# Kernel tuning notes

Hardware: AMD Instinct MI355X
Metric: run time of the kernel (lower is better)

Reference implementation:

```python
import jax, jax.numpy as jnp
import numpy as np

N = 50000   # nodes
E = 800000  # edges (avg degree 16)
D = 128     # node latent dim
DE = 128    # edge latent dim
L = 3       # num_mp_steps


def setup_inputs() -> dict:
    key = jax.random.key(0)
    ks = jax.random.split(key, 10)
    s = 0.05
    return dict(
        x=jax.random.normal(ks[0], (N, D), jnp.float32),
        edge_index=jax.random.randint(ks[1], (2, E), 0, N, jnp.int32),
        edge_attr=jax.random.normal(ks[2], (E, DE), jnp.float32),
        # per-layer GATConv params (stacked over L layers)
        W=jax.random.normal(ks[3], (L, D, D), jnp.float32) * s,        # lin (shared src/dst)
        att_src=jax.random.normal(ks[4], (L, D), jnp.float32) * s,
        att_dst=jax.random.normal(ks[5], (L, D), jnp.float32) * s,
        W_e=jax.random.normal(ks[6], (L, DE, D), jnp.float32) * s,     # lin_edge
        att_edge=jax.random.normal(ks[7], (L, D), jnp.float32) * s,
        bias=jnp.zeros((L, D), jnp.float32),
        ln_gamma=jnp.ones((L, D), jnp.float32),                        # post-conv LayerNorm
        ln_beta=jnp.zeros((L, D), jnp.float32),
    )


def reference(x, edge_index, edge_attr, W, att_src, att_dst, W_e, att_edge, bias, ln_gamma, ln_beta):
    n = x.shape[0]
    src, dst = edge_index[0], edge_index[1]

    # add_self_loops with fill_value='mean': self-loop edge feature of node i is
    # the mean of raw edge features of edges incoming to i (0 if none).
    ones = jnp.ones((src.shape[0],), x.dtype)
    deg = jax.ops.segment_sum(ones, dst, num_segments=n)
    loop_attr = jax.ops.segment_sum(edge_attr, dst, num_segments=n) / jnp.maximum(deg, 1.0)[:, None]
    loop = jnp.arange(n, dtype=src.dtype)
    src_f = jnp.concatenate([src, loop])            # [E+N]
    dst_f = jnp.concatenate([dst, loop])            # [E+N]
    ea_f = jnp.concatenate([edge_attr, loop_attr], axis=0)  # [E+N, DE]

    def layer(h_in, p):
        Wl, asl, adl, Wel, ael, bl, gl, bel = p
        h = h_in @ Wl                                              # [N, D]
        # per-edge attention logits (heads=1)
        a = (h @ asl)[src_f] + (h @ adl)[dst_f] + ea_f @ (Wel @ ael)  # [E+N]
        a = jnp.where(a > 0, a, 0.2 * a)                           # LeakyReLU(0.2)
        # segment softmax over destination nodes (every node has a self loop)
        m = jax.ops.segment_max(a, dst_f, num_segments=n)
        ea = jnp.exp(a - m[dst_f])
        denom = jax.ops.segment_sum(ea, dst_f, num_segments=n)
        alpha = ea / denom[dst_f]
        out = jax.ops.segment_sum(h[src_f] * alpha[:, None], dst_f, num_segments=n) + bl
        # LayerNorm (elementwise affine)
        mu = jnp.mean(out, axis=-1, keepdims=True)
        var = jnp.var(out, axis=-1, keepdims=True)
        out = (out - mu) * jax.lax.rsqrt(var + 1e-5) * gl + bel
        return out, None

    h, _ = jax.lax.scan(layer, x, (W, att_src, att_dst, W_e, att_edge, bias, ln_gamma, ln_beta))
    return h
```

## Files before the change

kernel.cpp:

```cpp
#include <hip/hip_runtime.h>
#include <cstdint>

#define D 128
#define LNUM 3

typedef short short8 __attribute__((ext_vector_type(8)));
typedef float f32x4 __attribute__((ext_vector_type(4)));

static __device__ __forceinline__ float wred_sum(float x) {
#pragma unroll
    for (int off = 32; off; off >>= 1) x += __shfl_xor(x, off);
    return x;
}
static __device__ __forceinline__ float wred_max(float x) {
#pragma unroll
    for (int off = 32; off; off >>= 1) x = fmaxf(x, __shfl_xor(x, off));
    return x;
}
static __device__ __forceinline__ uint32_t f2bf_rne(float x) {
    uint32_t u = __float_as_uint(x);
    uint32_t r = u + 0x7fffu + ((u >> 16) & 1u);
    return r >> 16;
}


__global__ void hist_k(const int* __restrict__ dst, int* __restrict__ cnt, int E) {
    int e = blockIdx.x * blockDim.x + threadIdx.x;
    if (e < E) atomicAdd(&cnt[dst[e]], 1);
}

__global__ __launch_bounds__(1024) void scan_k(const int* __restrict__ cnt, int* __restrict__ rowptr, int N) {
    __shared__ int sh[1024];
    int t = threadIdx.x;
    int chunk = (N + 1023) >> 10;
    int b = t * chunk;
    int e = min(b + chunk, N);
    int s = 0;
    for (int i = b; i < e; ++i) s += cnt[i];
    sh[t] = s;
    __syncthreads();
    for (int off = 1; off < 1024; off <<= 1) {
        int v = (t >= off) ? sh[t - off] : 0;
        __syncthreads();
        sh[t] += v;
        __syncthreads();
    }
    int run = sh[t] - s;
    for (int i = b; i < e; ++i) { rowptr[i] = run; run += cnt[i]; }
    if (t == 1023) rowptr[N] = sh[1023];
}

__global__ void fill_k(const int* __restrict__ src, const int* __restrict__ dst,
                       const int* __restrict__ rowptr, int* __restrict__ cnt,
                       int* __restrict__ colA, int* __restrict__ pos, int E) {
    int e = blockIdx.x * blockDim.x + threadIdx.x;
    if (e >= E) return;
    int d = dst[e];
    int p = atomicAdd(&cnt[d], 1);
    int q = rowptr[d] + p;
    colA[q] = src[e];
    pos[e] = q;
}


__global__ __launch_bounds__(256) void prep_k(const float* __restrict__ We, const float* __restrict__ ae,
                                              const float* __restrict__ W, float* __restrict__ vbuf,
                                              uint16_t* __restrict__ Wt) {
    int l = blockIdx.x;
    int t = threadIdx.x;
    if (t < D) {
        const float* Wrow = We + ((size_t)l * D + t) * D;
        const float* a = ae + (size_t)l * D;
        float s = 0.f;
        for (int d = 0; d < D; ++d) s += Wrow[d] * a[d];
        vbuf[l * D + t] = s;
    }
    for (int i = t; i < D * D; i += 256) {
        int j = i >> 7, k = i & 127;
        Wt[(size_t)l * D * D + i] = (uint16_t)f2bf_rne(W[(size_t)l * D * D + (size_t)k * D + j]);
    }
}


__global__ __launch_bounds__(256) void cvt_k(const float* __restrict__ x, uint16_t* __restrict__ xb, int total4) {
    int i = blockIdx.x * blockDim.x + threadIdx.x;
    int stride = gridDim.x * blockDim.x;
    for (; i < total4; i += stride) {
        float4 v = *(const float4*)&x[(size_t)i * 4];
        uint2 o;
        o.x = f2bf_rne(v.x) | (f2bf_rne(v.y) << 16);
        o.y = f2bf_rne(v.z) | (f2bf_rne(v.w) << 16);
        *(uint2*)&xb[(size_t)i * 4] = o;
    }
}


__global__ __launch_bounds__(256) void ec_k(const float* __restrict__ ea, const float* __restrict__ vbuf,
                                            const int* __restrict__ pos, float* __restrict__ ecp, int E) {
    __shared__ float vs[3][D];
    int t = threadIdx.x;
    if (t < D) {
        vs[0][t] = vbuf[t];
        vs[1][t] = vbuf[D + t];
        vs[2][t] = vbuf[2 * D + t];
    }
    __syncthreads();
    int e = blockIdx.x * 32 + (t >> 3);
    int sub = t & 7;
    if (e >= E) return;
    const float* row = ea + (size_t)e * D + sub * 16;
    float p0 = 0.f, p1 = 0.f, p2 = 0.f;
#pragma unroll
    for (int i = 0; i < 4; ++i) {
        float4 v = *(const float4*)&row[i * 4];
        int c = sub * 16 + i * 4;
        p0 += v.x * vs[0][c] + v.y * vs[0][c + 1] + v.z * vs[0][c + 2] + v.w * vs[0][c + 3];
        p1 += v.x * vs[1][c] + v.y * vs[1][c + 1] + v.z * vs[1][c + 2] + v.w * vs[1][c + 3];
        p2 += v.x * vs[2][c] + v.y * vs[2][c + 1] + v.z * vs[2][c + 2] + v.w * vs[2][c + 3];
    }
#pragma unroll
    for (int off = 1; off < 8; off <<= 1) {
        p0 += __shfl_xor(p0, off);
        p1 += __shfl_xor(p1, off);
        p2 += __shfl_xor(p2, off);
    }
    if (sub == 0) {
        int q = pos[e];
        ecp[q] = p0;
        ecp[E + q] = p1;
        ecp[2 * (size_t)E + q] = p2;
    }
}


__global__ __launch_bounds__(256) void gemm_mfma_k(const uint16_t* __restrict__ A,
                                                   const uint16_t* __restrict__ Wt,
                                                   const float* __restrict__ as_,
                                                   const float* __restrict__ ad_,
                                                   uint16_t* __restrict__ hbf,
                                                   float* __restrict__ hs, float* __restrict__ hd, int N) {
    __shared__ uint4 As[64 * 16];
    int t = threadIdx.x;
    int row0 = blockIdx.x * 64;
#pragma unroll
    for (int it = 0; it < 4; ++it) {
        int idx = it * 256 + t;
        int r = idx >> 4, s = idx & 15;
        int gr = row0 + r;
        uint4 v = make_uint4(0u, 0u, 0u, 0u);
        if (gr < N) v = *(const uint4*)&A[(size_t)gr * D + s * 8];
        As[r * 16 + (s ^ (r & 7))] = v;
    }
    __syncthreads();
    int w = t >> 6, l = t & 63;
    int lrow = l & 15, lk = l >> 4;
    int rbase = w * 16;
    short8 afrag[4];
#pragma unroll
    for (int ks = 0; ks < 4; ++ks) {
        int r = rbase + lrow;
        int s = (ks * 4 + lk) ^ (r & 7);
        afrag[ks] = __builtin_bit_cast(short8, As[r * 16 + s]);
    }
    float psum[4] = {0.f, 0.f, 0.f, 0.f}, pdum[4] = {0.f, 0.f, 0.f, 0.f};
#pragma unroll
    for (int ct = 0; ct < 8; ++ct) {
        f32x4 acc = {0.f, 0.f, 0.f, 0.f};
#pragma unroll
        for (int ks = 0; ks < 4; ++ks) {
            short8 b = *(const short8*)&Wt[(size_t)(ct * 16 + lrow) * D + ks * 32 + lk * 8];
            acc = __builtin_amdgcn_mfma_f32_16x16x32_bf16(afrag[ks], b, acc, 0, 0, 0);
        }
        int col_g = ct * 16 + lrow;
        float av = as_[col_g], dv = ad_[col_g];
#pragma unroll
        for (int r = 0; r < 4; ++r) {
            float v = acc[r];
            psum[r] += v * av;
            pdum[r] += v * dv;
            int row_g = row0 + rbase + lk * 4 + r;
            if (row_g < N) hbf[(size_t)row_g * D + col_g] = (uint16_t)f2bf_rne(v);
        }
    }
#pragma unroll
    for (int r = 0; r < 4; ++r) {
        float ps = psum[r], pd = pdum[r];
#pragma unroll
        for (int off = 1; off < 16; off <<= 1) {
            ps += __shfl_xor(ps, off);
            pd += __shfl_xor(pd, off);
        }
        if (lrow == 0) {
            int row_g = row0 + rbase + lk * 4 + r;
            if (row_g < N) { hs[row_g] = ps; hd[row_g] = pd; }
        }
    }
}


__global__ __launch_bounds__(256) void node_k(const uint32_t* __restrict__ hb, const float* __restrict__ hs,
                                              const float* __restrict__ hd, const float* __restrict__ ecp,
                                              const int* __restrict__ rowptr, const int* __restrict__ colA,
                                              const float* __restrict__ bias, const float* __restrict__ gamma,
                                              const float* __restrict__ beta,
                                              uint32_t* __restrict__ outb, float* __restrict__ outf, int N) {
    __shared__ float s_al[4][66];
    __shared__ int s_co[4][66];
    int w = threadIdx.x >> 6;
    int lane = threadIdx.x & 63;
    int wid = blockIdx.x * 4 + w;
    if (wid >= N) return;
    int beg = rowptr[wid], end = rowptr[wid + 1];
    int deg = end - beg;
    float hdi = hd[wid];
    float hsi = hs[wid];
    float acc0 = 0.f, acc1 = 0.f;

    if (deg <= 63) {
        bool v = lane < deg;
        int col = v ? colA[beg + lane] : 0;
        float ec = v ? ecp[beg + lane] : 0.f;
        float a = v ? (hs[col] + hdi + ec) : -3e38f;
        a = a > 0.f ? a : 0.2f * a;
        float sumec = wred_sum(ec);
        float ecs = deg > 0 ? sumec / (float)deg : 0.f;
        float as_ = hsi + hdi + ecs;
        as_ = as_ > 0.f ? as_ : 0.2f * as_;
        float m = fmaxf(wred_max(a), as_);
        float p = __expf(a - m);
        float ps = __expf(as_ - m);
        float denom = wred_sum(p) + ps;
        float inv = 1.f / denom;
        s_al[w][lane] = p * inv;
        s_co[w][lane] = col;
        if (lane == 0) { s_al[w][deg] = ps * inv; s_co[w][deg] = wid; }
        __asm__ volatile("s_waitcnt lgkmcnt(0)" ::: "memory");
        int ne = deg + 1;
        int j = 0;
        for (; j + 4 <= ne; j += 4) {
            int c0 = s_co[w][j], c1 = s_co[w][j + 1], c2 = s_co[w][j + 2], c3 = s_co[w][j + 3];
            float a0 = s_al[w][j], a1 = s_al[w][j + 1], a2 = s_al[w][j + 2], a3 = s_al[w][j + 3];
            uint32_t b0 = hb[(size_t)c0 * 64 + lane];
            uint32_t b1 = hb[(size_t)c1 * 64 + lane];
            uint32_t b2 = hb[(size_t)c2 * 64 + lane];
            uint32_t b3 = hb[(size_t)c3 * 64 + lane];
            acc0 += a0 * __uint_as_float(b0 << 16) + a1 * __uint_as_float(b1 << 16) +
                    a2 * __uint_as_float(b2 << 16) + a3 * __uint_as_float(b3 << 16);
            acc1 += a0 * __uint_as_float(b0 & 0xffff0000u) + a1 * __uint_as_float(b1 & 0xffff0000u) +
                    a2 * __uint_as_float(b2 & 0xffff0000u) + a3 * __uint_as_float(b3 & 0xffff0000u);
        }
        for (; j < ne; ++j) {
            int c0 = s_co[w][j];
            float a0 = s_al[w][j];
            uint32_t b0 = hb[(size_t)c0 * 64 + lane];
            acc0 += a0 * __uint_as_float(b0 << 16);
            acc1 += a0 * __uint_as_float(b0 & 0xffff0000u);
        }
    } else {
        float m = -3e38f, dsum = 0.f, sumec = 0.f;
        for (int base = 0; base < deg; base += 64) {
            int j = base + lane;
            bool v = j < deg;
            int col = v ? colA[beg + j] : 0;
            float ec = v ? ecp[beg + j] : 0.f;
            float a = v ? (hs[col] + hdi + ec) : -3e38f;
            a = a > 0.f ? a : 0.2f * a;
            sumec += wred_sum(ec);
            float cm = wred_max(a);
            float nm = fmaxf(m, cm);
            dsum = dsum * __expf(m - nm) + wred_sum(__expf(a - nm));
            m = nm;
        }
        float ecs = sumec / (float)deg;
        float as_ = hsi + hdi + ecs;
        as_ = as_ > 0.f ? as_ : 0.2f * as_;
        float nm = fmaxf(m, as_);
        dsum = dsum * __expf(m - nm) + __expf(as_ - nm);
        m = nm;
        float inv = 1.f / dsum;
        for (int base = 0; base < deg; base += 64) {
            int j = base + lane;
            bool v = j < deg;
            int col = v ? colA[beg + j] : 0;
            float ec = v ? ecp[beg + j] : 0.f;
            float a = v ? (hs[col] + hdi + ec) : -3e38f;
            a = a > 0.f ? a : 0.2f * a;
            __asm__ volatile("s_waitcnt lgkmcnt(0)" ::: "memory");
            s_al[w][lane] = __expf(a - m) * inv;
            s_co[w][lane] = col;
            __asm__ volatile("s_waitcnt lgkmcnt(0)" ::: "memory");
            int cnt = min(64, deg - base);
            for (int k = 0; k < cnt; ++k) {
                int c = s_co[w][k];
                float al = s_al[w][k];
                uint32_t b = hb[(size_t)c * 64 + lane];
                acc0 += al * __uint_as_float(b << 16);
                acc1 += al * __uint_as_float(b & 0xffff0000u);
            }
        }
        float alS = __expf(as_ - m) * inv;
        uint32_t b = hb[(size_t)wid * 64 + lane];
        acc0 += alS * __uint_as_float(b << 16);
        acc1 += alS * __uint_as_float(b & 0xffff0000u);
    }

    float2 bi = *(const float2*)&bias[lane * 2];
    float o0 = acc0 + bi.x, o1 = acc1 + bi.y;
    float mean = wred_sum(o0 + o1) * (1.f / 128.f);
    float d0 = o0 - mean, d1 = o1 - mean;
    float var = wred_sum(d0 * d0 + d1 * d1) * (1.f / 128.f);
    float rstd = rsqrtf(var + 1e-5f);
    float2 g = *(const float2*)&gamma[lane * 2];
    float2 be = *(const float2*)&beta[lane * 2];
    float2 o;
    o.x = d0 * rstd * g.x + be.x;
    o.y = d1 * rstd * g.y + be.y;
    if (outf) {
        *(float2*)&outf[(size_t)wid * D + lane * 2] = o;
    } else {
        outb[(size_t)wid * 64 + lane] = f2bf_rne(o.x) | (f2bf_rne(o.y) << 16);
    }
}


extern "C" void kernel_launch(void* const* d_in, const int* in_sizes, int n_in,
                              void* d_out, int out_size, void* d_ws, size_t ws_size,
                              hipStream_t stream) {
    const float* x = (const float*)d_in[0];
    const int* ei = (const int*)d_in[1];
    const float* ea = (const float*)d_in[2];
    const float* W = (const float*)d_in[3];
    const float* att_src = (const float*)d_in[4];
    const float* att_dst = (const float*)d_in[5];
    const float* We = (const float*)d_in[6];
    const float* att_edge = (const float*)d_in[7];
    const float* bias = (const float*)d_in[8];
    const float* gamma = (const float*)d_in[9];
    const float* beta = (const float*)d_in[10];

    int N = in_sizes[0] / D;
    int E = in_sizes[1] / 2;
    const int* srcA = ei;
    const int* dstA = ei + E;

    float* p = (float*)d_ws;
    float* hsb = p;   p += N;
    float* hdb = p;   p += N;
    float* vbuf = p;  p += LNUM * D;
    float* ecp = p;   p += (size_t)LNUM * E;
    uint16_t* xb = (uint16_t*)p;
    uint16_t* hbf = xb + (size_t)N * D;
    uint16_t* hnb = hbf + (size_t)N * D;
    uint16_t* Wt = hnb + (size_t)N * D;
    int* ip = (int*)(Wt + (size_t)LNUM * D * D);
    int* rowptr = ip; ip += N + 1;
    int* cnt = ip;    ip += N;
    int* colA = ip;   ip += E;
    int* pos = ip;    ip += E;

    hipMemsetAsync(cnt, 0, sizeof(int) * N, stream);
    hist_k<<<(E + 255) / 256, 256, 0, stream>>>(dstA, cnt, E);
    scan_k<<<1, 1024, 0, stream>>>(cnt, rowptr, N);
    hipMemsetAsync(cnt, 0, sizeof(int) * N, stream);
    fill_k<<<(E + 255) / 256, 256, 0, stream>>>(srcA, dstA, rowptr, cnt, colA, pos, E);
    prep_k<<<LNUM, 256, 0, stream>>>(We, att_edge, W, vbuf, Wt);
    ec_k<<<(E + 31) / 32, 256, 0, stream>>>(ea, vbuf, pos, ecp, E);
    cvt_k<<<2048, 256, 0, stream>>>(x, xb, N * D / 4);

    const uint16_t* hin = xb;
    for (int l = 0; l < LNUM; ++l) {
        gemm_mfma_k<<<(N + 63) / 64, 256, 0, stream>>>(hin, Wt + (size_t)l * D * D,
                                                       att_src + (size_t)l * D, att_dst + (size_t)l * D,
                                                       hbf, hsb, hdb, N);
        bool last = (l == LNUM - 1);
        node_k<<<(N + 3) / 4, 256, 0, stream>>>((const uint32_t*)hbf, hsb, hdb, ecp + (size_t)l * E,
                                                rowptr, colA, bias + (size_t)l * D,
                                                gamma + (size_t)l * D, beta + (size_t)l * D,
                                                last ? nullptr : (uint32_t*)hnb,
                                                last ? (float*)d_out : nullptr, N);
        hin = hnb;
    }
}
```

Before: 489.0 us.

## Fuse preprocessing kernels and pack CSR column with per-layer edge scores

Merges the histogram, weight transpose/convert, edge-vector projection and x-to-bf16 conversion into one grid-stride kernel. The CSR fill is folded into the edge-score kernel by decrementing the histogram counts with atomicSub, which removes the second memset and the pos array. Column index and the three per-layer edge logits are packed into one 16-byte record per edge, so node_k does a single vector load per edge. This cuts launches and the scattered writes, but each layer now reads 16 bytes per edge instead of 8.

Result: faster. 431.4 us (-11.8%).

```diff
diff --git a/kernel.cpp b/kernel.cpp
--- a/kernel.cpp
+++ b/kernel.cpp
@@ -24,10 +24,38 @@
 }
 
 
-__global__ void hist_k(const int* __restrict__ dst, int* __restrict__ cnt, int E) {
-    int e = blockIdx.x * blockDim.x + threadIdx.x;
-    if (e < E) atomicAdd(&cnt[dst[e]], 1);
-}
+__global__ __launch_bounds__(256) void pre_k(const float* __restrict__ W, const float* __restrict__ We,
+                                             const float* __restrict__ ae, const float* __restrict__ x,
+                                             const int* __restrict__ dst,
+                                             uint16_t* __restrict__ Wt, float* __restrict__ vbuf,
+                                             uint16_t* __restrict__ xb, int* __restrict__ cnt,
+                                             int ND4, int E) {
+    int tid = blockIdx.x * 256 + threadIdx.x;
+    int stride = gridDim.x * 256;
+    for (int i = tid; i < ND4; i += stride) {
+        float4 v = *(const float4*)&x[(size_t)i * 4];
+        uint2 o;
+        o.x = f2bf_rne(v.x) | (f2bf_rne(v.y) << 16);
+        o.y = f2bf_rne(v.z) | (f2bf_rne(v.w) << 16);
+        *(uint2*)&xb[(size_t)i * 4] = o;
+    }
+    for (int e = tid; e < E; e += stride) atomicAdd(&cnt[dst[e]], 1);
+    for (int i = tid; i < LNUM * D * D; i += stride) {
+        int l = i >> 14;
+        int r = i & (D * D - 1);
+        int j = r >> 7, k = r & 127;
+        Wt[i] = (uint16_t)f2bf_rne(W[(size_t)l * D * D + (size_t)k * D + j]);
+    }
+    if (tid < LNUM * D) {
+        int l = tid >> 7, j = tid & 127;
+        const float* Wrow = We + ((size_t)l * D + j) * D;
+        const float* a = ae + (size_t)l * D;
+        float s = 0.f;
+        for (int d = 0; d < D; ++d) s += Wrow[d] * a[d];
+        vbuf[tid] = s;
+    }
+}
+
 
 __global__ __launch_bounds__(1024) void scan_k(const int* __restrict__ cnt, int* __restrict__ rowptr, int N) {
     __shared__ int sh[1024];
@@ -50,53 +78,11 @@
     if (t == 1023) rowptr[N] = sh[1023];
 }
 
-__global__ void fill_k(const int* __restrict__ src, const int* __restrict__ dst,
-                       const int* __restrict__ rowptr, int* __restrict__ cnt,
-                       int* __restrict__ colA, int* __restrict__ pos, int E) {
-    int e = blockIdx.x * blockDim.x + threadIdx.x;
-    if (e >= E) return;
-    int d = dst[e];
-    int p = atomicAdd(&cnt[d], 1);
-    int q = rowptr[d] + p;
-    colA[q] = src[e];
-    pos[e] = q;
-}
-
-
-__global__ __launch_bounds__(256) void prep_k(const float* __restrict__ We, const float* __restrict__ ae,
-                                              const float* __restrict__ W, float* __restrict__ vbuf,
-                                              uint16_t* __restrict__ Wt) {
-    int l = blockIdx.x;
-    int t = threadIdx.x;
-    if (t < D) {
-        const float* Wrow = We + ((size_t)l * D + t) * D;
-        const float* a = ae + (size_t)l * D;
-        float s = 0.f;
-        for (int d = 0; d < D; ++d) s += Wrow[d] * a[d];
-        vbuf[l * D + t] = s;
-    }
-    for (int i = t; i < D * D; i += 256) {
-        int j = i >> 7, k = i & 127;
-        Wt[(size_t)l * D * D + i] = (uint16_t)f2bf_rne(W[(size_t)l * D * D + (size_t)k * D + j]);
-    }
-}
-
-
-__global__ __launch_bounds__(256) void cvt_k(const float* __restrict__ x, uint16_t* __restrict__ xb, int total4) {
-    int i = blockIdx.x * blockDim.x + threadIdx.x;
-    int stride = gridDim.x * blockDim.x;
-    for (; i < total4; i += stride) {
-        float4 v = *(const float4*)&x[(size_t)i * 4];
-        uint2 o;
-        o.x = f2bf_rne(v.x) | (f2bf_rne(v.y) << 16);
-        o.y = f2bf_rne(v.z) | (f2bf_rne(v.w) << 16);
-        *(uint2*)&xb[(size_t)i * 4] = o;
-    }
-}
-
-
-__global__ __launch_bounds__(256) void ec_k(const float* __restrict__ ea, const float* __restrict__ vbuf,
-                                            const int* __restrict__ pos, float* __restrict__ ecp, int E) {
+
+__global__ __launch_bounds__(256) void fillec_k(const float* __restrict__ ea, const float* __restrict__ vbuf,
+                                                const int* __restrict__ src, const int* __restrict__ dst,
+                                                const int* __restrict__ rowptr, int* __restrict__ cnt,
+                                                uint4* __restrict__ rec, int E) {
     __shared__ float vs[3][D];
     int t = threadIdx.x;
     if (t < D) {
@@ -125,10 +111,15 @@
         p2 += __shfl_xor(p2, off);
     }
     if (sub == 0) {
-        int q = pos[e];
-        ecp[q] = p0;
-        ecp[E + q] = p1;
-        ecp[2 * (size_t)E + q] = p2;
+        int d = dst[e];
+        int p = atomicSub(&cnt[d], 1) - 1;
+        int q = rowptr[d] + p;
+        uint4 r;
+        r.x = (uint32_t)src[e];
+        r.y = __float_as_uint(p0);
+        r.z = __float_as_uint(p1);
+        r.w = __float_as_uint(p2);
+        rec[q] = r;
     }
 }
 
@@ -199,11 +190,12 @@
 
 
 __global__ __launch_bounds__(256) void node_k(const uint32_t* __restrict__ hb, const float* __restrict__ hs,
-                                              const float* __restrict__ hd, const float* __restrict__ ecp,
-                                              const int* __restrict__ rowptr, const int* __restrict__ colA,
+                                              const float* __restrict__ hd, const uint4* __restrict__ rec,
+                                              const int* __restrict__ rowptr,
                                               const float* __restrict__ bias, const float* __restrict__ gamma,
                                               const float* __restrict__ beta,
-                                              uint32_t* __restrict__ outb, float* __restrict__ outf, int N) {
+                                              uint32_t* __restrict__ outb, float* __restrict__ outf,
+                                              int N, int lsel) {
     __shared__ float s_al[4][66];
     __shared__ int s_co[4][66];
     int w = threadIdx.x >> 6;
@@ -218,11 +210,13 @@
 
     if (deg <= 63) {
         bool v = lane < deg;
-        int col = v ? colA[beg + lane] : 0;
-        float ec = v ? ecp[beg + lane] : 0.f;
+        uint4 r = v ? rec[beg + lane] : make_uint4(0u, 0u, 0u, 0u);
+        int col = (int)r.x;
+        uint32_t ecu = lsel == 0 ? r.y : (lsel == 1 ? r.z : r.w);
+        float ec = __uint_as_float(ecu);
         float a = v ? (hs[col] + hdi + ec) : -3e38f;
         a = a > 0.f ? a : 0.2f * a;
-        float sumec = wred_sum(ec);
+        float sumec = wred_sum(v ? ec : 0.f);
         float ecs = deg > 0 ? sumec / (float)deg : 0.f;
         float as_ = hsi + hdi + ecs;
         as_ = as_ > 0.f ? as_ : 0.2f * as_;
@@ -259,13 +253,14 @@
     } else {
         float m = -3e38f, dsum = 0.f, sumec = 0.f;
         for (int base = 0; base < deg; base += 64) {
-            int j = base + lane;
-            bool v = j < deg;
-            int col = v ? colA[beg + j] : 0;
-            float ec = v ? ecp[beg + j] : 0.f;
-            float a = v ? (hs[col] + hdi + ec) : -3e38f;
+            int jj = base + lane;
+            bool v = jj < deg;
+            uint4 r = v ? rec[beg + jj] : make_uint4(0u, 0u, 0u, 0u);
+            uint32_t ecu = lsel == 0 ? r.y : (lsel == 1 ? r.z : r.w);
+            float ec = __uint_as_float(ecu);
+            float a = v ? (hs[(int)r.x] + hdi + ec) : -3e38f;
             a = a > 0.f ? a : 0.2f * a;
-            sumec += wred_sum(ec);
+            sumec += wred_sum(v ? ec : 0.f);
             float cm = wred_max(a);
             float nm = fmaxf(m, cm);
             dsum = dsum * __expf(m - nm) + wred_sum(__expf(a - nm));
@@ -279,10 +274,12 @@
         m = nm;
         float inv = 1.f / dsum;
         for (int base = 0; base < deg; base += 64) {
-            int j = base + lane;
-            bool v = j < deg;
-            int col = v ? colA[beg + j] : 0;
-            float ec = v ? ecp[beg + j] : 0.f;
+            int jj = base + lane;
+            bool v = jj < deg;
+            uint4 r = v ? rec[beg + jj] : make_uint4(0u, 0u, 0u, 0u);
+            int col = (int)r.x;
+            uint32_t ecu = lsel == 0 ? r.y : (lsel == 1 ? r.z : r.w);
+            float ec = __uint_as_float(ecu);
             float a = v ? (hs[col] + hdi + ec) : -3e38f;
             a = a > 0.f ? a : 0.2f * a;
             __asm__ volatile("s_waitcnt lgkmcnt(0)" ::: "memory");
@@ -347,25 +344,19 @@
     float* hsb = p;   p += N;
     float* hdb = p;   p += N;
     float* vbuf = p;  p += LNUM * D;
-    float* ecp = p;   p += (size_t)LNUM * E;
     uint16_t* xb = (uint16_t*)p;
     uint16_t* hbf = xb + (size_t)N * D;
     uint16_t* hnb = hbf + (size_t)N * D;
     uint16_t* Wt = hnb + (size_t)N * D;
-    int* ip = (int*)(Wt + (size_t)LNUM * D * D);
+    uint4* rec = (uint4*)(Wt + (size_t)LNUM * D * D);
+    int* ip = (int*)(rec + E);
     int* rowptr = ip; ip += N + 1;
     int* cnt = ip;    ip += N;
-    int* colA = ip;   ip += E;
-    int* pos = ip;    ip += E;
 
     hipMemsetAsync(cnt, 0, sizeof(int) * N, stream);
-    hist_k<<<(E + 255) / 256, 256, 0, stream>>>(dstA, cnt, E);
+    pre_k<<<1536, 256, 0, stream>>>(W, We, att_edge, x, dstA, Wt, vbuf, xb, cnt, N * D / 4, E);
     scan_k<<<1, 1024, 0, stream>>>(cnt, rowptr, N);
-    hipMemsetAsync(cnt, 0, sizeof(int) * N, stream);
-    fill_k<<<(E + 255) / 256, 256, 0, stream>>>(srcA, dstA, rowptr, cnt, colA, pos, E);
-    prep_k<<<LNUM, 256, 0, stream>>>(We, att_edge, W, vbuf, Wt);
-    ec_k<<<(E + 31) / 32, 256, 0, stream>>>(ea, vbuf, pos, ecp, E);
-    cvt_k<<<2048, 256, 0, stream>>>(x, xb, N * D / 4);
+    fillec_k<<<(E + 31) / 32, 256, 0, stream>>>(ea, vbuf, srcA, dstA, rowptr, cnt, rec, E);
 
     const uint16_t* hin = xb;
     for (int l = 0; l < LNUM; ++l) {
@@ -373,11 +364,11 @@
                                                        att_src + (size_t)l * D, att_dst + (size_t)l * D,
                                                        hbf, hsb, hdb, N);
         bool last = (l == LNUM - 1);
-        node_k<<<(N + 3) / 4, 256, 0, stream>>>((const uint32_t*)hbf, hsb, hdb, ecp + (size_t)l * E,
-                                                rowptr, colA, bias + (size_t)l * D,
-                                                gamma + (size_t)l * D, beta + (size_t)l * D,
+        node_k<<<(N + 3) / 4, 256, 0, stream>>>((const uint32_t*)hbf, hsb, hdb, rec, rowptr,
+                                                bias + (size_t)l * D, gamma + (size_t)l * D,
+                                                beta + (size_t)l * D,
                                                 last ? nullptr : (uint32_t*)hnb,
-                                                last ? (float*)d_out : nullptr, N);
+                                                last ? (float*)d_out : nullptr, N, l);
         hin = hnb;
     }
 }
```
